# Kernel tuning notes

Hardware: AMD Instinct MI355X
Metric: run time of the kernel (lower is better)

The kernel has to match this reference:

```python
import jax, jax.numpy as jnp
import numpy as np

B, N, NF, ND, NH = 16, 128, 64, 100, 64

def glorot(key, shape):
    fan_in, fan_out = shape[0], shape[1]
    limit = np.sqrt(6.0 / (fan_in + fan_out)).astype(np.float32)
    return jax.random.uniform(key, shape, jnp.float32, -limit, limit)

def setup_inputs() -> dict:
    key = jax.random.key(0)
    k1, k2, k3, k4, k5 = jax.random.split(key, 5)
    return {
        "atom_features": jax.random.normal(k1, (B, N, NF), jnp.float32),
        "distance_matrix": jax.random.uniform(k2, (B, N, N, ND), jnp.float32),
        "distance_matrix_mask": jnp.ones((B, N, N), jnp.float32),
        "W_cf": glorot(k3, (NF, NH)),
        "W_df": glorot(k4, (ND, NH)),
        "W_fc": glorot(k5, (NH, NF)),
        "b_cf": jnp.zeros((NH,), jnp.float32),
        "b_df": jnp.zeros((NH,), jnp.float32),
    }

def reference(atom_features, distance_matrix, distance_matrix_mask, W_cf, W_df, W_fc, b_cf, b_df):
    # dist_h: [B, N, N, H]
    dist_h = jnp.einsum('bijd,dh->bijh', distance_matrix, W_df) + b_df
    # atom_h: [B, N, H] -> broadcast over axis 1 (matches tf expand_dims axis=1)
    atom_h = jnp.einsum('bjf,fh->bjh', atom_features, W_cf) + b_cf
    gated = dist_h * atom_h[:, None, :, :]                 # [B, N, N, H]
    out = jnp.einsum('bijh,hf->bijf', gated, W_fc)          # [B, N, N, F]
    out = out * distance_matrix_mask[..., None]
    out = jnp.tanh(out)
    return jnp.sum(out, axis=2) + atom_features             # [B, N, F]
```

## Files before the change

### kernel.cpp

```cpp
#include <hip/hip_runtime.h>
#include <hip/hip_bf16.h>

#define Bsz 16
#define Nn  128
#define NFd 64
#define NDd 100
#define NHd 64

typedef __attribute__((ext_vector_type(8))) short bf16x8;
typedef __attribute__((ext_vector_type(4))) float f32x4;

__device__ __forceinline__ short f2bf(float f) {
  return (short)__builtin_bit_cast(ushort, __float2bfloat16(f));
}

__device__ __forceinline__ float fast_tanh(float x) {
  float e = __expf(2.0f * x);
  return 1.0f - 2.0f * __builtin_amdgcn_rcpf(e + 1.0f);
}

__device__ __forceinline__ void glds16(const float* g, float* l) {
  __builtin_amdgcn_global_load_lds(
      (const __attribute__((address_space(1))) void*)g,
      (__attribute__((address_space(3))) void*)l, 16, 0, 0);
}
__device__ __forceinline__ void glds4(const float* g, float* l) {
  __builtin_amdgcn_global_load_lds(
      (const __attribute__((address_space(1))) void*)g,
      (__attribute__((address_space(3))) void*)l, 4, 0, 0);
}

__global__ __launch_bounds__(256) void prep_kernel(
    const float* __restrict__ AF, const float* __restrict__ Wcf,
    const float* __restrict__ bcf, const float* __restrict__ Wdf,
    const float* __restrict__ Wfc, float* __restrict__ atomhT,
    ushort* __restrict__ wdfp, ushort* __restrict__ wfcp,
    float* __restrict__ out) {
  int t = threadIdx.x;
  int blk = blockIdx.x;
  if (blk < 512) {
    int row = blk * 4 + (t >> 6);
    int h = t & 63;
    const float* af = AF + (size_t)row * NFd;
    float a0 = 0.f, a1 = 0.f, a2 = 0.f, a3 = 0.f;
    #pragma unroll 4
    for (int f = 0; f < NFd; f += 4) {
      a0 += af[f + 0] * Wcf[(f + 0) * NHd + h];
      a1 += af[f + 1] * Wcf[(f + 1) * NHd + h];
      a2 += af[f + 2] * Wcf[(f + 2) * NHd + h];
      a3 += af[f + 3] * Wcf[(f + 3) * NHd + h];
    }
    int b = row >> 7, j = row & 127;
    atomhT[((size_t)(b * NHd + h)) << 7 | j] = bcf[h] + ((a0 + a1) + (a2 + a3));
    out[(size_t)row * NFd + h] = af[h];
  } else if (blk < 544) {
    int idx = (blk - 512) * 256 + t;
    int e = idx & 7;
    int col = (idx >> 3) & 63;
    int grp = idx >> 9;
    int k = grp * 8 + e;
    float v = (k < NDd) ? Wdf[k * NHd + col] : 0.f;
    wdfp[idx] = (ushort)f2bf(v);
  } else {
    int idx = (blk - 544) * 256 + t;
    int e = idx & 7;
    int col = (idx >> 3) & 63;
    int grp = idx >> 9;
    int k = grp * 8 + e;
    wfcp[idx] = (ushort)f2bf(Wfc[k * NFd + col]);
  }
}

__global__ __launch_bounds__(256, 4) void dtnn_main_kernel(
    const float* __restrict__ DM,
    const float* __restrict__ MASK,
    const float* __restrict__ bdf,
    const float* __restrict__ atomhT,
    const ushort* __restrict__ wdfp,
    const ushort* __restrict__ wfcp,
    float* __restrict__ out) {
  __shared__ float stage[4 * 1600];

  const int t    = threadIdx.x;
  const int blk  = blockIdx.x;
  const int bi   = blk >> 1;
  const int half = blk & 1;
  const int b    = bi >> 7;
  const int w    = t >> 6;
  const int lane = t & 63;
  const int p    = t & 15;
  const int q    = (t >> 4) & 3;

  const int jrow = half * 64 + w * 16;

  const float* gsrc = DM + (size_t)bi * (Nn * NDd) + (size_t)jrow * NDd;
  float* lb = stage + w * 1600;
  {
    const int r8 = lane >> 3, b8 = lane & 7;
    #pragma unroll
    for (int c = 0; c < 3; ++c) {
      #pragma unroll
      for (int g = 0; g < 2; ++g) {
        int r = g * 8 + r8;
        glds16(gsrc + r * 100 + c * 32 + ((b8 ^ (r & 7)) << 2),
               lb + c * 512 + g * 256);
      }
    }
    glds4(gsrc + (lane >> 2) * 100 + 96 + (lane & 3), lb + 1536);
  }

  const bf16x8* wdfv = reinterpret_cast<const bf16x8*>(wdfp);
  const bf16x8* wfcv = reinterpret_cast<const bf16x8*>(wfcp);

  f32x4 ah[4];
  #pragma unroll
  for (int ht = 0; ht < 4; ++ht)
    ah[ht] = *reinterpret_cast<const f32x4*>(
        atomhT + (((size_t)(b * NHd + ht * 16 + p)) << 7) + jrow + 4 * q);
  f32x4 mv = *reinterpret_cast<const f32x4*>(MASK + (size_t)bi * Nn + jrow + 4 * q);
  float bv[4];
  #pragma unroll
  for (int ht = 0; ht < 4; ++ht) bv[ht] = bdf[ht * 16 + p];

  asm volatile("s_waitcnt vmcnt(0)" ::: "memory");
  __builtin_amdgcn_sched_barrier(0);

  f32x4 acc[4];
  #pragma unroll
  for (int ht = 0; ht < 4; ++ht) acc[ht] = (f32x4){bv[ht], bv[ht], bv[ht], bv[ht]};

  #pragma unroll
  for (int ks = 0; ks < 3; ++ks) {
    const float* cbase = lb + ks * 512 + p * 32;
    f32x4 x = *reinterpret_cast<const f32x4*>(cbase + (((2 * q)     ) ^ (p & 7)) * 4);
    f32x4 y = *reinterpret_cast<const f32x4*>(cbase + (((2 * q) + 1 ) ^ (p & 7)) * 4);
    bf16x8 a;
    a[0] = f2bf(x[0]); a[1] = f2bf(x[1]); a[2] = f2bf(x[2]); a[3] = f2bf(x[3]);
    a[4] = f2bf(y[0]); a[5] = f2bf(y[1]); a[6] = f2bf(y[2]); a[7] = f2bf(y[3]);
    #pragma unroll
    for (int ht = 0; ht < 4; ++ht)
      acc[ht] = __builtin_amdgcn_mfma_f32_16x16x32_bf16(
          a, wdfv[(ks * 4 + q) * 64 + ht * 16 + p], acc[ht], 0, 0, 0);
  }
  {
    bf16x8 a = (bf16x8){0, 0, 0, 0, 0, 0, 0, 0};
    if (q == 0) {
      f32x4 tx = *reinterpret_cast<const f32x4*>(lb + 1536 + 4 * p);
      a[0] = f2bf(tx[0]); a[1] = f2bf(tx[1]); a[2] = f2bf(tx[2]); a[3] = f2bf(tx[3]);
    }
    #pragma unroll
    for (int ht = 0; ht < 4; ++ht)
      acc[ht] = __builtin_amdgcn_mfma_f32_16x16x32_bf16(
          a, wdfv[(12 + q) * 64 + ht * 16 + p], acc[ht], 0, 0, 0);
  }

  #pragma unroll
  for (int ht = 0; ht < 4; ++ht) {
    #pragma unroll
    for (int r = 0; r < 4; ++r) acc[ht][r] *= ah[ht][r];
  }

  ushort* gb = reinterpret_cast<ushort*>(lb);
  #pragma unroll
  for (int r = 0; r < 4; ++r) {
    int rr = 4 * q + r;
    int sw = (rr & 7) << 3;
    #pragma unroll
    for (int ht = 0; ht < 4; ++ht)
      gb[rr * 64 + ((ht * 16 + p) ^ sw)] = (ushort)f2bf(acc[ht][r]);
  }
  asm volatile("" ::: "memory");

  f32x4 acc2[4];
  #pragma unroll
  for (int ft = 0; ft < 4; ++ft) acc2[ft] = (f32x4){0.f, 0.f, 0.f, 0.f};

  #pragma unroll
  for (int ks = 0; ks < 2; ++ks) {
    int h0 = (ks * 32 + q * 8) ^ ((p & 7) << 3);
    bf16x8 a2 = *reinterpret_cast<const bf16x8*>(&gb[p * 64 + h0]);
    #pragma unroll
    for (int ft = 0; ft < 4; ++ft)
      acc2[ft] = __builtin_amdgcn_mfma_f32_16x16x32_bf16(
          a2, wfcv[(ks * 4 + q) * 64 + ft * 16 + p], acc2[ft], 0, 0, 0);
  }

  float s[4] = {0.f, 0.f, 0.f, 0.f};
  #pragma unroll
  for (int r = 0; r < 4; ++r) {
    #pragma unroll
    for (int ft = 0; ft < 4; ++ft) s[ft] += fast_tanh(acc2[ft][r] * mv[r]);
  }

  #pragma unroll
  for (int ft = 0; ft < 4; ++ft) {
    s[ft] += __shfl_xor(s[ft], 16, 64);
    s[ft] += __shfl_xor(s[ft], 32, 64);
  }
  if (q == 0) {
    #pragma unroll
    for (int ft = 0; ft < 4; ++ft)
      unsafeAtomicAdd(&out[(size_t)bi * NFd + ft * 16 + p], s[ft]);
  }
}

extern "C" void kernel_launch(void* const* d_in, const int* in_sizes, int n_in,
                              void* d_out, int out_size, void* d_ws, size_t ws_size,
                              hipStream_t stream) {
  const float* AF   = (const float*)d_in[0];
  const float* DM   = (const float*)d_in[1];
  const float* MASK = (const float*)d_in[2];
  const float* Wcf  = (const float*)d_in[3];
  const float* Wdf  = (const float*)d_in[4];
  const float* Wfc  = (const float*)d_in[5];
  const float* bcf  = (const float*)d_in[6];
  const float* bdf  = (const float*)d_in[7];
  float* out = (float*)d_out;

  float*  atomhT = (float*)d_ws;
  ushort* wdfp   = (ushort*)((char*)d_ws + 524288);
  ushort* wfcp   = (ushort*)((char*)d_ws + 524288 + 16384);

  prep_kernel<<<560, 256, 0, stream>>>(AF, Wcf, bcf, Wdf, Wfc, atomhT, wdfp, wfcp, out);
  dtnn_main_kernel<<<2 * Bsz * Nn, 256, 0, stream>>>(DM, MASK, bdf, atomhT, wdfp, wfcp, out);
}
```

Measured before the change: 41.65 us.

## Give each wave a full output row with double-buffered DM loads and LDS weights

The main kernel now assigns one (b,i) row per wave, looping over 8 chunks of 16 j-rows with double-buffered async global-to-LDS loads so the next chunk's fetch overlaps the current chunk's MFMAs. Both packed bf16 weight matrices are staged once per block in LDS instead of being read from global memory per fragment. Because each row is reduced entirely by one wave, the atomic adds and the residual copy in the prep kernel are replaced by a direct store of sum plus atom features. The grid drops to 512 blocks and occupancy is lowered to 2 blocks per SIMD-set, which cuts parallelism and the number of loads in flight.

```diff
diff --git a/kernel.cpp b/kernel.cpp
--- a/kernel.cpp
+++ b/kernel.cpp
@@ -34,8 +34,7 @@
     const float* __restrict__ AF, const float* __restrict__ Wcf,
     const float* __restrict__ bcf, const float* __restrict__ Wdf,
     const float* __restrict__ Wfc, float* __restrict__ atomhT,
-    ushort* __restrict__ wdfp, ushort* __restrict__ wfcp,
-    float* __restrict__ out) {
+    ushort* __restrict__ wdfp, ushort* __restrict__ wfcp) {
   int t = threadIdx.x;
   int blk = blockIdx.x;
   if (blk < 512) {
@@ -52,7 +51,6 @@
     }
     int b = row >> 7, j = row & 127;
     atomhT[((size_t)(b * NHd + h)) << 7 | j] = bcf[h] + ((a0 + a1) + (a2 + a3));
-    out[(size_t)row * NFd + h] = af[h];
   } else if (blk < 544) {
     int idx = (blk - 512) * 256 + t;
     int e = idx & 7;
@@ -71,7 +69,8 @@
   }
 }
 
-__global__ __launch_bounds__(256, 4) void dtnn_main_kernel(
+__global__ __launch_bounds__(256, 2) void dtnn_main_kernel(
+    const float* __restrict__ AF,
     const float* __restrict__ DM,
     const float* __restrict__ MASK,
     const float* __restrict__ bdf,
@@ -79,24 +78,48 @@
     const ushort* __restrict__ wdfp,
     const ushort* __restrict__ wfcp,
     float* __restrict__ out) {
-  __shared__ float stage[4 * 1600];
+  __shared__ float  stage[4 * 2 * 1600];
+  __shared__ ushort wdf_lds[8192];
+  __shared__ ushort wfc_lds[4096];
 
   const int t    = threadIdx.x;
-  const int blk  = blockIdx.x;
-  const int bi   = blk >> 1;
-  const int half = blk & 1;
-  const int b    = bi >> 7;
   const int w    = t >> 6;
   const int lane = t & 63;
   const int p    = t & 15;
   const int q    = (t >> 4) & 3;
 
-  const int jrow = half * 64 + w * 16;
-
-  const float* gsrc = DM + (size_t)bi * (Nn * NDd) + (size_t)jrow * NDd;
-  float* lb = stage + w * 1600;
+  const int bi = blockIdx.x * 4 + w;
+  const int b  = bi >> 7;
+
   {
-    const int r8 = lane >> 3, b8 = lane & 7;
+    const float* wsrc = (const float*)wdfp;
+    float* wdst = reinterpret_cast<float*>(wdf_lds);
+    #pragma unroll
+    for (int m = 0; m < 4; ++m) {
+      int k = w + 4 * m;
+      glds16(wsrc + k * 256 + lane * 4, wdst + k * 256);
+    }
+    const float* fsrc = (const float*)wfcp;
+    float* fdst = reinterpret_cast<float*>(wfc_lds);
+    #pragma unroll
+    for (int m = 0; m < 2; ++m) {
+      int k = w + 4 * m;
+      glds16(fsrc + k * 256 + lane * 4, fdst + k * 256);
+    }
+  }
+
+  float bv[4];
+  #pragma unroll
+  for (int ht = 0; ht < 4; ++ht) bv[ht] = bdf[ht * 16 + p];
+
+  const float* gD = DM + (size_t)bi * (Nn * NDd);
+  f32x4 ah[2][4];
+  f32x4 mv[2];
+  const int r8 = lane >> 3, b8 = lane & 7;
+
+  auto ISSUE = [&](int n) {
+    const float* gsrc = gD + n * 1600;
+    float* lb = &stage[w * 3200 + (n & 1) * 1600];
     #pragma unroll
     for (int c = 0; c < 3; ++c) {
       #pragma unroll
@@ -107,89 +130,101 @@
       }
     }
     glds4(gsrc + (lane >> 2) * 100 + 96 + (lane & 3), lb + 1536);
-  }
-
-  const bf16x8* wdfv = reinterpret_cast<const bf16x8*>(wdfp);
-  const bf16x8* wfcv = reinterpret_cast<const bf16x8*>(wfcp);
-
-  f32x4 ah[4];
+    const int jrow = n * 16;
+    #pragma unroll
+    for (int ht = 0; ht < 4; ++ht)
+      ah[n & 1][ht] = *reinterpret_cast<const f32x4*>(
+          atomhT + (((size_t)(b * NHd + ht * 16 + p)) << 7) + jrow + 4 * q);
+    mv[n & 1] = *reinterpret_cast<const f32x4*>(MASK + (size_t)bi * Nn + jrow + 4 * q);
+  };
+
+  ISSUE(0);
+  __syncthreads();
+
+  float s[4] = {0.f, 0.f, 0.f, 0.f};
+
   #pragma unroll
-  for (int ht = 0; ht < 4; ++ht)
-    ah[ht] = *reinterpret_cast<const f32x4*>(
-        atomhT + (((size_t)(b * NHd + ht * 16 + p)) << 7) + jrow + 4 * q);
-  f32x4 mv = *reinterpret_cast<const f32x4*>(MASK + (size_t)bi * Nn + jrow + 4 * q);
-  float bv[4];
-  #pragma unroll
-  for (int ht = 0; ht < 4; ++ht) bv[ht] = bdf[ht * 16 + p];
-
-  asm volatile("s_waitcnt vmcnt(0)" ::: "memory");
-  __builtin_amdgcn_sched_barrier(0);
-
-  f32x4 acc[4];
-  #pragma unroll
-  for (int ht = 0; ht < 4; ++ht) acc[ht] = (f32x4){bv[ht], bv[ht], bv[ht], bv[ht]};
-
-  #pragma unroll
-  for (int ks = 0; ks < 3; ++ks) {
-    const float* cbase = lb + ks * 512 + p * 32;
-    f32x4 x = *reinterpret_cast<const f32x4*>(cbase + (((2 * q)     ) ^ (p & 7)) * 4);
-    f32x4 y = *reinterpret_cast<const f32x4*>(cbase + (((2 * q) + 1 ) ^ (p & 7)) * 4);
-    bf16x8 a;
-    a[0] = f2bf(x[0]); a[1] = f2bf(x[1]); a[2] = f2bf(x[2]); a[3] = f2bf(x[3]);
-    a[4] = f2bf(y[0]); a[5] = f2bf(y[1]); a[6] = f2bf(y[2]); a[7] = f2bf(y[3]);
-    #pragma unroll
-    for (int ht = 0; ht < 4; ++ht)
-      acc[ht] = __builtin_amdgcn_mfma_f32_16x16x32_bf16(
-          a, wdfv[(ks * 4 + q) * 64 + ht * 16 + p], acc[ht], 0, 0, 0);
-  }
-  {
-    bf16x8 a = (bf16x8){0, 0, 0, 0, 0, 0, 0, 0};
-    if (q == 0) {
-      f32x4 tx = *reinterpret_cast<const f32x4*>(lb + 1536 + 4 * p);
-      a[0] = f2bf(tx[0]); a[1] = f2bf(tx[1]); a[2] = f2bf(tx[2]); a[3] = f2bf(tx[3]);
-    }
-    #pragma unroll
-    for (int ht = 0; ht < 4; ++ht)
-      acc[ht] = __builtin_amdgcn_mfma_f32_16x16x32_bf16(
-          a, wdfv[(12 + q) * 64 + ht * 16 + p], acc[ht], 0, 0, 0);
-  }
-
-  #pragma unroll
-  for (int ht = 0; ht < 4; ++ht) {
-    #pragma unroll
-    for (int r = 0; r < 4; ++r) acc[ht][r] *= ah[ht][r];
-  }
-
-  ushort* gb = reinterpret_cast<ushort*>(lb);
-  #pragma unroll
-  for (int r = 0; r < 4; ++r) {
-    int rr = 4 * q + r;
-    int sw = (rr & 7) << 3;
-    #pragma unroll
-    for (int ht = 0; ht < 4; ++ht)
-      gb[rr * 64 + ((ht * 16 + p) ^ sw)] = (ushort)f2bf(acc[ht][r]);
-  }
-  asm volatile("" ::: "memory");
-
-  f32x4 acc2[4];
-  #pragma unroll
-  for (int ft = 0; ft < 4; ++ft) acc2[ft] = (f32x4){0.f, 0.f, 0.f, 0.f};
-
-  #pragma unroll
-  for (int ks = 0; ks < 2; ++ks) {
-    int h0 = (ks * 32 + q * 8) ^ ((p & 7) << 3);
-    bf16x8 a2 = *reinterpret_cast<const bf16x8*>(&gb[p * 64 + h0]);
-    #pragma unroll
-    for (int ft = 0; ft < 4; ++ft)
-      acc2[ft] = __builtin_amdgcn_mfma_f32_16x16x32_bf16(
-          a2, wfcv[(ks * 4 + q) * 64 + ft * 16 + p], acc2[ft], 0, 0, 0);
-  }
-
-  float s[4] = {0.f, 0.f, 0.f, 0.f};
-  #pragma unroll
-  for (int r = 0; r < 4; ++r) {
-    #pragma unroll
-    for (int ft = 0; ft < 4; ++ft) s[ft] += fast_tanh(acc2[ft][r] * mv[r]);
+  for (int n = 0; n < 8; ++n) {
+    if (n < 7) {
+      ISSUE(n + 1);
+      asm volatile("s_waitcnt vmcnt(12)" ::: "memory");
+    } else {
+      asm volatile("s_waitcnt vmcnt(0)" ::: "memory");
+    }
+    __builtin_amdgcn_sched_barrier(0);
+
+    float* lb = &stage[w * 3200 + (n & 1) * 1600];
+
+    f32x4 acc[4];
+    #pragma unroll
+    for (int ht = 0; ht < 4; ++ht) acc[ht] = (f32x4){bv[ht], bv[ht], bv[ht], bv[ht]};
+
+    #pragma unroll
+    for (int ks = 0; ks < 3; ++ks) {
+      const float* cbase = lb + ks * 512 + p * 32;
+      f32x4 x = *reinterpret_cast<const f32x4*>(cbase + (((2 * q)    ) ^ (p & 7)) * 4);
+      f32x4 y = *reinterpret_cast<const f32x4*>(cbase + (((2 * q) + 1) ^ (p & 7)) * 4);
+      bf16x8 a;
+      a[0] = f2bf(x[0]); a[1] = f2bf(x[1]); a[2] = f2bf(x[2]); a[3] = f2bf(x[3]);
+      a[4] = f2bf(y[0]); a[5] = f2bf(y[1]); a[6] = f2bf(y[2]); a[7] = f2bf(y[3]);
+      #pragma unroll
+      for (int ht = 0; ht < 4; ++ht) {
+        bf16x8 bfr = *reinterpret_cast<const bf16x8*>(
+            &wdf_lds[((ks * 4 + q) * 64 + ht * 16 + p) * 8]);
+        acc[ht] = __builtin_amdgcn_mfma_f32_16x16x32_bf16(a, bfr, acc[ht], 0, 0, 0);
+      }
+    }
+    {
+      bf16x8 a = (bf16x8){0, 0, 0, 0, 0, 0, 0, 0};
+      if (q == 0) {
+        f32x4 tx = *reinterpret_cast<const f32x4*>(lb + 1536 + 4 * p);
+        a[0] = f2bf(tx[0]); a[1] = f2bf(tx[1]); a[2] = f2bf(tx[2]); a[3] = f2bf(tx[3]);
+      }
+      #pragma unroll
+      for (int ht = 0; ht < 4; ++ht) {
+        bf16x8 bfr = *reinterpret_cast<const bf16x8*>(
+            &wdf_lds[((12 + q) * 64 + ht * 16 + p) * 8]);
+        acc[ht] = __builtin_amdgcn_mfma_f32_16x16x32_bf16(a, bfr, acc[ht], 0, 0, 0);
+      }
+    }
+
+    #pragma unroll
+    for (int ht = 0; ht < 4; ++ht) {
+      #pragma unroll
+      for (int r = 0; r < 4; ++r) acc[ht][r] *= ah[n & 1][ht][r];
+    }
+
+    ushort* gb = reinterpret_cast<ushort*>(lb);
+    #pragma unroll
+    for (int r = 0; r < 4; ++r) {
+      int rr = 4 * q + r;
+      int sw = (rr & 7) << 3;
+      #pragma unroll
+      for (int ht = 0; ht < 4; ++ht)
+        gb[rr * 64 + ((ht * 16 + p) ^ sw)] = (ushort)f2bf(acc[ht][r]);
+    }
+    asm volatile("" ::: "memory");
+
+    f32x4 acc2[4];
+    #pragma unroll
+    for (int ft = 0; ft < 4; ++ft) acc2[ft] = (f32x4){0.f, 0.f, 0.f, 0.f};
+    #pragma unroll
+    for (int ks = 0; ks < 2; ++ks) {
+      int h0 = (ks * 32 + q * 8) ^ ((p & 7) << 3);
+      bf16x8 a2 = *reinterpret_cast<const bf16x8*>(&gb[p * 64 + h0]);
+      #pragma unroll
+      for (int ft = 0; ft < 4; ++ft) {
+        bf16x8 bfr = *reinterpret_cast<const bf16x8*>(
+            &wfc_lds[((ks * 4 + q) * 64 + ft * 16 + p) * 8]);
+        acc2[ft] = __builtin_amdgcn_mfma_f32_16x16x32_bf16(a2, bfr, acc2[ft], 0, 0, 0);
+      }
+    }
+
+    #pragma unroll
+    for (int r = 0; r < 4; ++r) {
+      #pragma unroll
+      for (int ft = 0; ft < 4; ++ft) s[ft] += fast_tanh(acc2[ft][r] * mv[n & 1][r]);
+    }
   }
 
   #pragma unroll
@@ -199,8 +234,10 @@
   }
   if (q == 0) {
     #pragma unroll
-    for (int ft = 0; ft < 4; ++ft)
-      unsafeAtomicAdd(&out[(size_t)bi * NFd + ft * 16 + p], s[ft]);
+    for (int ft = 0; ft < 4; ++ft) {
+      int o = bi * NFd + ft * 16 + p;
+      out[o] = s[ft] + AF[o];
+    }
   }
 }
 
@@ -221,6 +258,6 @@
   ushort* wdfp   = (ushort*)((char*)d_ws + 524288);
   ushort* wfcp   = (ushort*)((char*)d_ws + 524288 + 16384);
 
-  prep_kernel<<<560, 256, 0, stream>>>(AF, Wcf, bcf, Wdf, Wfc, atomhT, wdfp, wfcp, out);
-  dtnn_main_kernel<<<2 * Bsz * Nn, 256, 0, stream>>>(DM, MASK, bdf, atomhT, wdfp, wfcp, out);
-}
+  prep_kernel<<<560, 256, 0, stream>>>(AF, Wcf, bcf, Wdf, Wfc, atomhT, wdfp, wfcp);
+  dtnn_main_kernel<<<512, 256, 0, stream>>>(AF, DM, MASK, bdf, atomhT, wdfp, wfcp, out);
+}
```

Measured after the change: 33.99 us (median of 4 runs). 18.4% less time.
